# Performance work log

Hardware: AMD Instinct MI355X
Metric: run time of the kernel (lower is better)

## Reference

```python
import jax, jax.numpy as jnp
import numpy as np

NUM_NEURONS = 256
NUM_SAMPLES = 512
MAX_SPIKES = 32
N_STEPS = 32          # fixed RK4 steps per spike round (stands in for adaptive Tsit5)
ALPHA = 0.03
V_RESET = 1.0
T0 = 0.0


def setup_inputs() -> dict:
    key = jax.random.key(0)
    ks = jax.random.split(key, 7)
    input_current = jax.random.normal(ks[0], (NUM_NEURONS,), dtype=jnp.float32)
    # _build_w with network=all-False: uniform(minval=0.5), mask sets nothing
    w = jax.random.uniform(ks[1], (NUM_NEURONS, NUM_NEURONS), minval=0.5, maxval=1.0, dtype=jnp.float32)
    mu = jax.random.uniform(ks[2], (2,), minval=0.5, maxval=1.0, dtype=jnp.float32)
    v0 = jax.random.normal(ks[3], (NUM_NEURONS,), dtype=jnp.float32)
    i0 = jax.random.normal(ks[4], (NUM_NEURONS,), dtype=jnp.float32)
    # s0 = log(U) - alpha  (always < 0)
    s0 = (jnp.log(jax.random.uniform(ks[5], (NUM_SAMPLES, NUM_NEURONS), minval=1e-6, maxval=1.0)) - ALPHA).astype(jnp.float32)
    # pre-drawn stochastic resets, one per (spike round, sample, neuron)
    reset_s = (jnp.log(jax.random.uniform(ks[6], (MAX_SPIKES, NUM_SAMPLES, NUM_NEURONS), minval=1e-6, maxval=1.0)) - ALPHA).astype(jnp.float32)
    return dict(input_current=input_current, w=w, mu=mu, v0=v0, i0=i0, s0=s0, reset_s=reset_s, t1=2)


def _drift(y, ic, mu1, mu2):
    # y: [samples, neurons, 3] = (v, i, s)
    v, i = y[..., 0], y[..., 1]
    dv = mu1 * (i + ic - v)
    di = -mu2 * i
    ds = jax.nn.sigmoid(v)  # intensity_fn(v)
    return jnp.stack([dv, di, ds], axis=-1)


def reference(input_current, w, mu, v0, i0, s0, reset_s, t1):
    t1f = jnp.float32(t1)
    mu1, mu2 = mu[0], mu[1]
    ic = input_current  # constant-in-time input current, [neurons]

    y0 = jnp.concatenate([
        jnp.broadcast_to(v0, (NUM_SAMPLES, NUM_NEURONS))[..., None],
        jnp.broadcast_to(i0, (NUM_SAMPLES, NUM_NEURONS))[..., None],
        s0[..., None]], axis=-1)  # [samples, neurons, 3]

    def rk4(y, h):
        k1 = _drift(y, ic, mu1, mu2)
        k2 = _drift(y + 0.5 * h * k1, ic, mu1, mu2)
        k3 = _drift(y + 0.5 * h * k2, ic, mu1, mu2)
        k4 = _drift(y + h * k3, ic, mu1, mu2)
        return y + (h / 6.0) * (k1 + 2.0 * k2 + 2.0 * k3 + k4)

    def round_body(carry, reset_k):
        t0s, y_in = carry                      # t0s: [samples]
        dt = (t1f - t0s) / N_STEPS             # per-sample step size
        h = dt[:, None, None]

        def step(sc, _):
            t, y, done, tev, yev, emask = sc
            y_new = rk4(y, h)
            y_new = jnp.where(done[:, None, None], y, y_new)  # freeze after event
            s_prev, s_new = y[..., 2], y_new[..., 2]
            crossed = s_new > 0.0                              # cond_fn root: s crosses 0
            trig = crossed.any(axis=1) & (~done)
            idx = jnp.argmax(s_new, axis=1)                    # event neuron (first/largest crossing)
            sp = jnp.take_along_axis(s_prev, idx[:, None], 1)[:, 0]
            sn = jnp.take_along_axis(s_new, idx[:, None], 1)[:, 0]
            frac = jnp.clip(sp / (sp - sn + 1e-12), 0.0, 1.0)  # linear root estimate (Newton stand-in)
            t_c = t + frac * dt
            y_c = y + frac[:, None, None] * (y_new - y)
            tev = jnp.where(trig, t_c, tev)
            yev = jnp.where(trig[:, None, None], y_c, yev)
            emask = jnp.where(trig[:, None], crossed, emask)
            y = jnp.where(trig[:, None, None], y_c, y_new)
            done = done | trig
            return (t + dt, y, done, tev, yev, emask), None

        done0 = jnp.zeros((NUM_SAMPLES,), bool)
        tev0 = jnp.full((NUM_SAMPLES,), jnp.inf, jnp.float32)
        em0 = jnp.zeros((NUM_SAMPLES, NUM_NEURONS), bool)
        (_, yend, done, tev, yev, emask), _ = jax.lax.scan(
            step, (t0s, y_in, done0, tev0, y_in, em0), None, length=N_STEPS)

        tev = jnp.where(done, tev, t1f)                 # no event -> sol.ts[-1] = t1
        yev = jnp.where(done[:, None, None], yev, yend)

        # trans_fn: spike reset + synaptic jump w[event_idx]
        eidx = jnp.argmax(emask, axis=1)
        w_row = jnp.where(done[:, None], w[eidx], 0.0)  # zero if no event happened
        v_t = yev[..., 0] - jnp.where(emask, V_RESET, 0.0)
        i_t = yev[..., 1] + w_row
        s_t = jnp.minimum(jnp.where(emask, reset_k, yev[..., 2]), 0.0)
        y_next = jnp.stack([v_t, i_t, s_t], axis=-1)
        return (tev, y_next), (tev, yev, emask)

    t0s = jnp.full((NUM_SAMPLES,), T0, jnp.float32)
    _, (tevs, yevs, emasks) = jax.lax.scan(jax.checkpoint(round_body), (t0s, y0), reset_s)

    spike_times = jnp.transpose(tevs, (1, 0))            # [samples, max_spikes]
    spike_values = jnp.transpose(yevs, (1, 0, 2, 3))     # [samples, max_spikes, neurons, 3]
    spike_marks = jnp.transpose(emasks, (1, 0, 2))       # [samples, max_spikes, neurons]
    return spike_times, spike_values, spike_marks
```

## Files before the change

kernel.cpp:

```cpp
#include <hip/hip_runtime.h>
#include <math.h>

#define NN 256
#define NS 512
#define MS 32
#define NSTEP 32
#define VRESET 1.0f

__device__ __forceinline__ float sigf(float x) {
    float e = __expf(-x);
    return __builtin_amdgcn_rcpf(1.0f + e);
}

__device__ __forceinline__ void block_sync_lds() {
    asm volatile("s_waitcnt lgkmcnt(0)" ::: "memory");
    __builtin_amdgcn_s_barrier();
    asm volatile("" ::: "memory");
}

__device__ __forceinline__ void rk4step(float v, float ii, float s,
                                        float ic, float mu1, float mu2,
                                        float dt, float hh, float h6,
                                        float& vn, float& in_, float& sn)
{
    float kv1 = mu1 * (ii + ic - v);
    float ki1 = -mu2 * ii;
    float ks1 = sigf(v);
    float v2 = v + hh * kv1;
    float i2 = ii + hh * ki1;
    float kv2 = mu1 * (i2 + ic - v2);
    float ki2 = -mu2 * i2;
    float ks2 = sigf(v2);
    float v3 = v + hh * kv2;
    float i3 = ii + hh * ki2;
    float kv3 = mu1 * (i3 + ic - v3);
    float ki3 = -mu2 * i3;
    float ks3 = sigf(v3);
    float v4 = v + dt * kv3;
    float i4 = ii + dt * ki3;
    float kv4 = mu1 * (i4 + ic - v4);
    float ki4 = -mu2 * i4;
    float ks4 = sigf(v4);
    vn  = v  + h6 * (kv1 + 2.0f * kv2 + 2.0f * kv3 + kv4);
    in_ = ii + h6 * (ki1 + 2.0f * ki2 + 2.0f * ki3 + ki4);
    sn  = s  + h6 * (ks1 + 2.0f * ks2 + 2.0f * ks3 + ks4);
}

__global__ __launch_bounds__(256) void snn_kernel(
    const float* __restrict__ ic_g,
    const float* __restrict__ w,
    const float* __restrict__ mu,
    const float* __restrict__ v0,
    const float* __restrict__ i0,
    const float* __restrict__ s0,
    const float* __restrict__ reset_s,
    const int*   __restrict__ t1p,
    float* __restrict__ out)
{
    const int tid  = threadIdx.x;
    const int lane = tid & 63;
    const int wid  = tid >> 6;
    const int samp = blockIdx.x;
    const float mu1 = mu[0];
    const float mu2 = mu[1];
    const float t1f = (float)t1p[0];

    __shared__ int   s_any[4][4];
    __shared__ float s_sn[NN];
    __shared__ float s_sp[NN];
    __shared__ unsigned long long s_key[4];
    __shared__ int   s_eidx[4];

    float v  = v0[tid];
    float ii = i0[tid];
    float s  = s0[samp * NN + tid];
    const float ic = ic_g[tid];
    float t0 = 0.0f;

    float* times = out;
    float* vals  = out + (size_t)NS * MS;
    float* marks = out + (size_t)NS * MS * (1 + NN * 3);

    for (int r = 0; r < MS; ++r) {
        const float rs = reset_s[((size_t)r * NS + samp) * NN + tid];

        const float dt = (t1f - t0) / (float)NSTEP;
        float tev = t1f;
        float yv = v, yi = ii, ys = s;
        bool  em = false;
        bool  done = false;
        float wr = 0.0f;

        if (dt != 0.0f) {
            const float hh = 0.5f * dt;
            const float h6 = dt * (1.0f / 6.0f);

            float pv = v, pi_ = ii, ps = s;
            float cv, ci, cs;
            rk4step(pv, pi_, ps, ic, mu1, mu2, dt, hh, h6, cv, ci, cs);
            float t = t0;

            for (int st = 0; st < NSTEP; ++st) {
                unsigned long long bl = __ballot(cs > 0.0f);
                if (lane == 0) s_any[st & 3][wid] = (bl != 0ull) ? 1 : 0;

                float nv = 0.0f, ni = 0.0f, ns_ = 0.0f;
                const bool notlast = (st + 1 < NSTEP);
                if (notlast)
                    rk4step(cv, ci, cs, ic, mu1, mu2, dt, hh, h6, nv, ni, ns_);

                block_sync_lds();
                int af = s_any[st & 3][0] | s_any[st & 3][1] |
                         s_any[st & 3][2] | s_any[st & 3][3];

                if (af) {
                    bool crossed = cs > 0.0f;
                    s_sn[tid] = cs;
                    s_sp[tid] = ps;

                    unsigned int b = __float_as_uint(cs);
                    unsigned int m = (b & 0x80000000u) ? 0xFFFFFFFFu : 0x80000000u;
                    unsigned long long key =
                        ((unsigned long long)(b ^ m) << 32) |
                        (unsigned int)(NN - 1 - tid);
#pragma unroll
                    for (int off = 32; off >= 1; off >>= 1) {
                        unsigned long long o = __shfl_xor(key, off);
                        key = (o > key) ? o : key;
                    }
                    unsigned long long bm = __ballot(crossed);
                    int cand = (bm != 0ull)
                                   ? (wid * 64 + (int)__builtin_ctzll(bm))
                                   : (2 * NN);
                    if (lane == 0) { s_key[wid] = key; s_eidx[wid] = cand; }
                    block_sync_lds();

                    unsigned long long k0 = s_key[0], k1 = s_key[1];
                    unsigned long long k2 = s_key[2], k3 = s_key[3];
                    k0 = (k1 > k0) ? k1 : k0;
                    k2 = (k3 > k2) ? k3 : k2;
                    k0 = (k2 > k0) ? k2 : k0;
                    int bn = NN - 1 - (int)(unsigned int)(k0 & 0xFFFFFFFFull);

                    int eidx = s_eidx[0];
                    eidx = (s_eidx[1] < eidx) ? s_eidx[1] : eidx;
                    eidx = (s_eidx[2] < eidx) ? s_eidx[2] : eidx;
                    eidx = (s_eidx[3] < eidx) ? s_eidx[3] : eidx;

                    wr = w[eidx * NN + tid];

                    float bv  = s_sn[bn];
                    float bsp = s_sp[bn];
                    float frac = bsp / (bsp - bv + 1e-12f);
                    frac = fminf(fmaxf(frac, 0.0f), 1.0f);
                    tev = t + frac * dt;
                    yv = pv  + frac * (cv - pv);
                    yi = pi_ + frac * (ci - pi_);
                    ys = ps  + frac * (cs - ps);
                    em = crossed;
                    done = true;
                    break;
                }

                if (notlast) {
                    pv = cv; pi_ = ci; ps = cs;
                    cv = nv; ci = ni; cs = ns_;
                    t += dt;
                }
            }

            if (!done) { yv = cv; yi = ci; ys = cs; }
        }

        const int sr = samp * MS + r;
        if (tid == 0) times[sr] = tev;
        {
            float* p = vals + ((size_t)sr * NN + tid) * 3;
            p[0] = yv;
            p[1] = yi;
            p[2] = ys;
            marks[(size_t)sr * NN + tid] = em ? 1.0f : 0.0f;
        }

        if (done) {
            v  = yv - (em ? VRESET : 0.0f);
            ii = yi + wr;
            float sres = em ? rs : ys;
            s = fminf(sres, 0.0f);
        } else {
            v = yv; ii = yi;
            s = fminf(ys, 0.0f);
        }
        t0 = tev;
    }
}

extern "C" void kernel_launch(void* const* d_in, const int* in_sizes, int n_in,
                              void* d_out, int out_size, void* d_ws, size_t ws_size,
                              hipStream_t stream) {
    const float* ic      = (const float*)d_in[0];
    const float* w       = (const float*)d_in[1];
    const float* mu      = (const float*)d_in[2];
    const float* v0      = (const float*)d_in[3];
    const float* i0      = (const float*)d_in[4];
    const float* s0      = (const float*)d_in[5];
    const float* reset_s = (const float*)d_in[6];
    const int*   t1p     = (const int*)d_in[7];
    float* out = (float*)d_out;

    snn_kernel<<<dim3(NS), dim3(256), 0, stream>>>(ic, w, mu, v0, i0, s0,
                                                   reset_s, t1p, out);
}
```

Baseline: 143.6 us.

## Batch spike-detection barriers over four RK4 steps with speculative lookahead

Instead of one block-wide barrier per RK4 step to check whether any neuron has crossed threshold, the loop now computes four steps at a time, packs the four per-wave ballot results into a bitmask, and synchronises once per window. Two steps of the next window are computed speculatively around the barrier to hide its latency. On detection, the first crossing step is chosen from the mask and the same interpolation runs as before. This cuts barriers roughly fourfold, at the cost of more live registers and wasted speculative RK4 work when a spike occurs early in a window.

Measured after the change: 163.7 us. +14.0%, slower.

```diff
diff --git a/kernel.cpp b/kernel.cpp
--- a/kernel.cpp
+++ b/kernel.cpp
@@ -65,7 +65,7 @@
     const float mu2 = mu[1];
     const float t1f = (float)t1p[0];
 
-    __shared__ int   s_any[4][4];
+    __shared__ int4  s_any4[2];
     __shared__ float s_sn[NN];
     __shared__ float s_sp[NN];
     __shared__ unsigned long long s_key[4];
@@ -95,33 +95,65 @@
             const float hh = 0.5f * dt;
             const float h6 = dt * (1.0f / 6.0f);
 
-            float pv = v, pi_ = ii, ps = s;
-            float cv, ci, cs;
-            rk4step(pv, pi_, ps, ic, mu1, mu2, dt, hh, h6, cv, ci, cs);
-            float t = t0;
-
-            for (int st = 0; st < NSTEP; ++st) {
-                unsigned long long bl = __ballot(cs > 0.0f);
-                if (lane == 0) s_any[st & 3][wid] = (bl != 0ull) ? 1 : 0;
-
-                float nv = 0.0f, ni = 0.0f, ns_ = 0.0f;
-                const bool notlast = (st + 1 < NSTEP);
-                if (notlast)
-                    rk4step(cv, ci, cs, ic, mu1, mu2, dt, hh, h6, nv, ni, ns_);
-
+            float w0v = v, w0i = ii, w0s = s;
+            float w1v, w1i, w1s, w2v, w2i, w2s;
+            float w3v, w3i, w3s, w4v, w4i, w4s;
+            rk4step(w0v, w0i, w0s, ic, mu1, mu2, dt, hh, h6, w1v, w1i, w1s);
+            rk4step(w1v, w1i, w1s, ic, mu1, mu2, dt, hh, h6, w2v, w2i, w2s);
+            float tw = t0;
+
+            for (int wdx = 0; wdx < NSTEP / 4; ++wdx) {
+                rk4step(w2v, w2i, w2s, ic, mu1, mu2, dt, hh, h6, w3v, w3i, w3s);
+                rk4step(w3v, w3i, w3s, ic, mu1, mu2, dt, hh, h6, w4v, w4i, w4s);
+
+                unsigned long long b1 = __ballot(w1s > 0.0f);
+                unsigned long long b2 = __ballot(w2s > 0.0f);
+                unsigned long long b3 = __ballot(w3s > 0.0f);
+                unsigned long long b4 = __ballot(w4s > 0.0f);
+                int m = (b1 ? 1 : 0) | (b2 ? 2 : 0) | (b3 ? 4 : 0) | (b4 ? 8 : 0);
+                if (lane == 0) ((int*)&s_any4[wdx & 1])[wid] = m;
+
+                const bool spec = (wdx < NSTEP / 4 - 1);
+                float n1v = 0.0f, n1i = 0.0f, n1s = 0.0f;
+                float n2v = 0.0f, n2i = 0.0f, n2s = 0.0f;
+                if (spec)
+                    rk4step(w4v, w4i, w4s, ic, mu1, mu2, dt, hh, h6,
+                            n1v, n1i, n1s);
+
+                __builtin_amdgcn_sched_barrier(0);
                 block_sync_lds();
-                int af = s_any[st & 3][0] | s_any[st & 3][1] |
-                         s_any[st & 3][2] | s_any[st & 3][3];
-
-                if (af) {
-                    bool crossed = cs > 0.0f;
-                    s_sn[tid] = cs;
+                __builtin_amdgcn_sched_barrier(0);
+
+                int4 fl = s_any4[wdx & 1];
+                if (spec)
+                    rk4step(n1v, n1i, n1s, ic, mu1, mu2, dt, hh, h6,
+                            n2v, n2i, n2s);
+
+                int mAll = fl.x | fl.y | fl.z | fl.w;
+
+                if (mAll) {
+                    int j = __builtin_ctz((unsigned)mAll) + 1;
+                    float pv, pi_, ps, cvv, cii, css;
+                    if (j == 1)      { pv = w0v; pi_ = w0i; ps = w0s;
+                                       cvv = w1v; cii = w1i; css = w1s; }
+                    else if (j == 2) { pv = w1v; pi_ = w1i; ps = w1s;
+                                       cvv = w2v; cii = w2i; css = w2s; }
+                    else if (j == 3) { pv = w2v; pi_ = w2i; ps = w2s;
+                                       cvv = w3v; cii = w3i; css = w3s; }
+                    else             { pv = w3v; pi_ = w3i; ps = w3s;
+                                       cvv = w4v; cii = w4i; css = w4s; }
+                    float te = tw;
+                    for (int q = 1; q < j; ++q) te += dt;
+
+                    bool crossed = css > 0.0f;
+                    s_sn[tid] = css;
                     s_sp[tid] = ps;
 
-                    unsigned int b = __float_as_uint(cs);
-                    unsigned int m = (b & 0x80000000u) ? 0xFFFFFFFFu : 0x80000000u;
+                    unsigned int b = __float_as_uint(css);
+                    unsigned int msk = (b & 0x80000000u) ? 0xFFFFFFFFu
+                                                         : 0x80000000u;
                     unsigned long long key =
-                        ((unsigned long long)(b ^ m) << 32) |
+                        ((unsigned long long)(b ^ msk) << 32) |
                         (unsigned int)(NN - 1 - tid);
 #pragma unroll
                     for (int off = 32; off >= 1; off >>= 1) {
@@ -153,23 +185,24 @@
                     float bsp = s_sp[bn];
                     float frac = bsp / (bsp - bv + 1e-12f);
                     frac = fminf(fmaxf(frac, 0.0f), 1.0f);
-                    tev = t + frac * dt;
-                    yv = pv  + frac * (cv - pv);
-                    yi = pi_ + frac * (ci - pi_);
-                    ys = ps  + frac * (cs - ps);
+                    tev = te + frac * dt;
+                    yv = pv  + frac * (cvv - pv);
+                    yi = pi_ + frac * (cii - pi_);
+                    ys = ps  + frac * (css - ps);
                     em = crossed;
                     done = true;
                     break;
                 }
 
-                if (notlast) {
-                    pv = cv; pi_ = ci; ps = cs;
-                    cv = nv; ci = ni; cs = ns_;
-                    t += dt;
+                if (spec) {
+                    w0v = w4v; w0i = w4i; w0s = w4s;
+                    w1v = n1v; w1i = n1i; w1s = n1s;
+                    w2v = n2v; w2i = n2i; w2s = n2s;
+                    tw += dt; tw += dt; tw += dt; tw += dt;
                 }
             }
 
-            if (!done) { yv = cv; yi = ci; ys = cs; }
+            if (!done) { yv = w4v; yi = w4i; ys = w4s; }
         }
 
         const int sr = samp * MS + r;
```

## Replace per-step block barrier with LDS mailbox and two-step lookahead

Applied to the files above, without the earlier changes.

Drops the workgroup barrier on every RK4 step. Each wavefront now posts a step-tagged crossing flag into an LDS mailbox and runs up to two steps ahead before polling, with s_sleep, for the other wavefronts' flags. It keeps a three-deep history of states so the event interval can be rebuilt once a crossing is seen. The aim is to hide barrier latency behind RK4 arithmetic. The cost is spin-polling on volatile LDS, more register pressure, and reliance on LDS visibility ordering between wavefronts without a fence.

New measurement: 159.1 us. 10.8% more time.

```diff
diff --git a/kernel.cpp b/kernel.cpp
--- a/kernel.cpp
+++ b/kernel.cpp
@@ -65,11 +65,14 @@
     const float mu2 = mu[1];
     const float t1f = (float)t1p[0];
 
-    __shared__ int   s_any[4][4];
+    __shared__ int4  mb4[NSTEP + 1];
     __shared__ float s_sn[NN];
     __shared__ float s_sp[NN];
     __shared__ unsigned long long s_key[4];
     __shared__ int   s_eidx[4];
+
+    if (tid < NSTEP + 1) mb4[tid] = make_int4(0, 0, 0, 0);
+    __syncthreads();
 
     float v  = v0[tid];
     float ii = i0[tid];
@@ -90,86 +93,148 @@
         bool  em = false;
         bool  done = false;
         float wr = 0.0f;
+        float te = t0;
+        float ev_pv = 0.f, ev_pi = 0.f, ev_ps = 0.f;
+        float ev_cv = 0.f, ev_ci = 0.f, ev_cs = 0.f;
 
         if (dt != 0.0f) {
             const float hh = 0.5f * dt;
             const float h6 = dt * (1.0f / 6.0f);
-
-            float pv = v, pi_ = ii, ps = s;
-            float cv, ci, cs;
-            rk4step(pv, pi_, ps, ic, mu1, mu2, dt, hh, h6, cv, ci, cs);
-            float t = t0;
-
-            for (int st = 0; st < NSTEP; ++st) {
-                unsigned long long bl = __ballot(cs > 0.0f);
-                if (lane == 0) s_any[st & 3][wid] = (bl != 0ull) ? 1 : 0;
-
-                float nv = 0.0f, ni = 0.0f, ns_ = 0.0f;
-                const bool notlast = (st + 1 < NSTEP);
-                if (notlast)
-                    rk4step(cv, ci, cs, ic, mu1, mu2, dt, hh, h6, nv, ni, ns_);
-
-                block_sync_lds();
-                int af = s_any[st & 3][0] | s_any[st & 3][1] |
-                         s_any[st & 3][2] | s_any[st & 3][3];
-
-                if (af) {
-                    bool crossed = cs > 0.0f;
-                    s_sn[tid] = cs;
-                    s_sp[tid] = ps;
-
-                    unsigned int b = __float_as_uint(cs);
-                    unsigned int m = (b & 0x80000000u) ? 0xFFFFFFFFu : 0x80000000u;
-                    unsigned long long key =
-                        ((unsigned long long)(b ^ m) << 32) |
-                        (unsigned int)(NN - 1 - tid);
+            const int keybase = r * (NSTEP + 1);
+
+            float Av = 0.f, Ai = 0.f, As = 0.f;
+            float Bv = 0.f, Bi = 0.f, Bs = 0.f;
+            float Pv = v, Pi = ii, Ps = s;
+            float Cv, Ci, Cs;
+
 #pragma unroll
-                    for (int off = 32; off >= 1; off >>= 1) {
-                        unsigned long long o = __shfl_xor(key, off);
-                        key = (o > key) ? o : key;
-                    }
-                    unsigned long long bm = __ballot(crossed);
-                    int cand = (bm != 0ull)
-                                   ? (wid * 64 + (int)__builtin_ctzll(bm))
-                                   : (2 * NN);
-                    if (lane == 0) { s_key[wid] = key; s_eidx[wid] = cand; }
-                    block_sync_lds();
-
-                    unsigned long long k0 = s_key[0], k1 = s_key[1];
-                    unsigned long long k2 = s_key[2], k3 = s_key[3];
-                    k0 = (k1 > k0) ? k1 : k0;
-                    k2 = (k3 > k2) ? k3 : k2;
-                    k0 = (k2 > k0) ? k2 : k0;
-                    int bn = NN - 1 - (int)(unsigned int)(k0 & 0xFFFFFFFFull);
-
-                    int eidx = s_eidx[0];
-                    eidx = (s_eidx[1] < eidx) ? s_eidx[1] : eidx;
-                    eidx = (s_eidx[2] < eidx) ? s_eidx[2] : eidx;
-                    eidx = (s_eidx[3] < eidx) ? s_eidx[3] : eidx;
-
-                    wr = w[eidx * NN + tid];
-
-                    float bv  = s_sn[bn];
-                    float bsp = s_sp[bn];
-                    float frac = bsp / (bsp - bv + 1e-12f);
-                    frac = fminf(fmaxf(frac, 0.0f), 1.0f);
-                    tev = t + frac * dt;
-                    yv = pv  + frac * (cv - pv);
-                    yi = pi_ + frac * (ci - pi_);
-                    ys = ps  + frac * (cs - ps);
-                    em = crossed;
+            for (int st = 1; st <= 2; ++st) {
+                rk4step(Pv, Pi, Ps, ic, mu1, mu2, dt, hh, h6, Cv, Ci, Cs);
+                unsigned long long bl = __ballot(Cs > 0.0f);
+                int val = ((keybase + st) << 1) | ((bl != 0ull) ? 1 : 0);
+                if (lane == 0) ((volatile int*)&mb4[st])[wid] = val;
+                Av = Bv; Ai = Bi; As = Bs;
+                Bv = Pv; Bi = Pi; Bs = Ps;
+                Pv = Cv; Pi = Ci; Ps = Cs;
+            }
+
+            for (int st = 3; st <= NSTEP; ++st) {
+                const int slot = st - 2;
+                volatile int* mbr = (volatile int*)&mb4[slot];
+                int f0 = mbr[0], f1 = mbr[1], f2 = mbr[2], f3 = mbr[3];
+
+                rk4step(Pv, Pi, Ps, ic, mu1, mu2, dt, hh, h6, Cv, Ci, Cs);
+
+                unsigned long long bl = __ballot(Cs > 0.0f);
+                int val = ((keybase + st) << 1) | ((bl != 0ull) ? 1 : 0);
+                if (lane == 0) ((volatile int*)&mb4[st])[wid] = val;
+
+                const int key = keybase + slot;
+                while (!(((f0 >> 1) == key) & ((f1 >> 1) == key) &
+                         ((f2 >> 1) == key) & ((f3 >> 1) == key))) {
+                    __builtin_amdgcn_s_sleep(1);
+                    f0 = mbr[0]; f1 = mbr[1]; f2 = mbr[2]; f3 = mbr[3];
+                }
+                if (((f0 | f1 | f2 | f3) & 1) != 0) {
+                    ev_pv = Av; ev_pi = Ai; ev_ps = As;
+                    ev_cv = Bv; ev_ci = Bi; ev_cs = Bs;
                     done = true;
                     break;
                 }
-
-                if (notlast) {
-                    pv = cv; pi_ = ci; ps = cs;
-                    cv = nv; ci = ni; cs = ns_;
-                    t += dt;
-                }
-            }
-
-            if (!done) { yv = cv; yi = ci; ys = cs; }
+                te += dt;
+
+                Av = Bv; Ai = Bi; As = Bs;
+                Bv = Pv; Bi = Pi; Bs = Ps;
+                Pv = Cv; Pi = Ci; Ps = Cs;
+            }
+
+            if (!done) {
+                {
+                    const int slot = NSTEP - 1;
+                    const int key = keybase + slot;
+                    volatile int* mbr = (volatile int*)&mb4[slot];
+                    int f0 = mbr[0], f1 = mbr[1], f2 = mbr[2], f3 = mbr[3];
+                    while (!(((f0 >> 1) == key) & ((f1 >> 1) == key) &
+                             ((f2 >> 1) == key) & ((f3 >> 1) == key))) {
+                        __builtin_amdgcn_s_sleep(1);
+                        f0 = mbr[0]; f1 = mbr[1]; f2 = mbr[2]; f3 = mbr[3];
+                    }
+                    if (((f0 | f1 | f2 | f3) & 1) != 0) {
+                        ev_pv = Av; ev_pi = Ai; ev_ps = As;
+                        ev_cv = Bv; ev_ci = Bi; ev_cs = Bs;
+                        done = true;
+                    } else {
+                        te += dt;
+                    }
+                }
+                if (!done) {
+                    const int slot = NSTEP;
+                    const int key = keybase + slot;
+                    volatile int* mbr = (volatile int*)&mb4[slot];
+                    int f0 = mbr[0], f1 = mbr[1], f2 = mbr[2], f3 = mbr[3];
+                    while (!(((f0 >> 1) == key) & ((f1 >> 1) == key) &
+                             ((f2 >> 1) == key) & ((f3 >> 1) == key))) {
+                        __builtin_amdgcn_s_sleep(1);
+                        f0 = mbr[0]; f1 = mbr[1]; f2 = mbr[2]; f3 = mbr[3];
+                    }
+                    if (((f0 | f1 | f2 | f3) & 1) != 0) {
+                        ev_pv = Bv; ev_pi = Bi; ev_ps = Bs;
+                        ev_cv = Pv; ev_ci = Pi; ev_cs = Ps;
+                        done = true;
+                    }
+                }
+            }
+
+            if (done) {
+                bool crossed = ev_cs > 0.0f;
+                s_sn[tid] = ev_cs;
+                s_sp[tid] = ev_ps;
+
+                unsigned int b = __float_as_uint(ev_cs);
+                unsigned int msk = (b & 0x80000000u) ? 0xFFFFFFFFu
+                                                     : 0x80000000u;
+                unsigned long long key =
+                    ((unsigned long long)(b ^ msk) << 32) |
+                    (unsigned int)(NN - 1 - tid);
+#pragma unroll
+                for (int off = 32; off >= 1; off >>= 1) {
+                    unsigned long long o = __shfl_xor(key, off);
+                    key = (o > key) ? o : key;
+                }
+                unsigned long long bm = __ballot(crossed);
+                int cand = (bm != 0ull)
+                               ? (wid * 64 + (int)__builtin_ctzll(bm))
+                               : (2 * NN);
+                if (lane == 0) { s_key[wid] = key; s_eidx[wid] = cand; }
+                block_sync_lds();
+
+                unsigned long long k0 = s_key[0], k1 = s_key[1];
+                unsigned long long k2 = s_key[2], k3 = s_key[3];
+                k0 = (k1 > k0) ? k1 : k0;
+                k2 = (k3 > k2) ? k3 : k2;
+                k0 = (k2 > k0) ? k2 : k0;
+                int bn = NN - 1 - (int)(unsigned int)(k0 & 0xFFFFFFFFull);
+
+                int eidx = s_eidx[0];
+                eidx = (s_eidx[1] < eidx) ? s_eidx[1] : eidx;
+                eidx = (s_eidx[2] < eidx) ? s_eidx[2] : eidx;
+                eidx = (s_eidx[3] < eidx) ? s_eidx[3] : eidx;
+
+                wr = w[eidx * NN + tid];
+
+                float bv  = s_sn[bn];
+                float bsp = s_sp[bn];
+                float frac = bsp / (bsp - bv + 1e-12f);
+                frac = fminf(fmaxf(frac, 0.0f), 1.0f);
+                tev = te + frac * dt;
+                yv = ev_pv + frac * (ev_cv - ev_pv);
+                yi = ev_pi + frac * (ev_ci - ev_pi);
+                ys = ev_ps + frac * (ev_cs - ev_ps);
+                em = crossed;
+            } else {
+                yv = Pv; yi = Pi; ys = Ps;
+                block_sync_lds();
+            }
         }
 
         const int sr = samp * MS + r;
```
